# Kernel optimization log

Hardware: AMD Instinct MI355X
Metric: run time of the kernel (lower is better)

## Reference

```python
import jax, jax.numpy as jnp
import numpy as np

B, S, H, I = 2, 2048, 4096, 16384
EPS = 1e-12


def setup_inputs() -> dict:
    key = jax.random.key(0)
    ks = jax.random.split(key, 8)
    w_scale = 0.02
    return {
        "input": jax.random.normal(ks[0], (B, S, H), jnp.float32),
        "residual": jax.random.normal(ks[1], (B, S, H), jnp.float32),
        "bias": jax.random.normal(ks[2], (H,), jnp.float32) * w_scale,
        "attn_nw": jnp.ones((H,), jnp.float32),
        "attn_nb": jnp.zeros((H,), jnp.float32),
        "inter_w": jax.random.normal(ks[3], (I, H), jnp.float32) * w_scale,
        "inter_b": jax.random.normal(ks[4], (I,), jnp.float32) * w_scale,
        "output_w": jax.random.normal(ks[5], (H, I), jnp.float32) * w_scale,
        "output_b": jax.random.normal(ks[6], (H,), jnp.float32) * w_scale,
    }


def reference(input, residual, bias, attn_nw, attn_nb, inter_w, inter_b, output_w, output_b):
    # Fused mlp_gemm: residual_add = input + residual + attn-output bias
    residual_add = input + residual + bias  # [B,S,H]
    # LayerNorm over hidden dim with attn_nw/attn_nb
    mean = jnp.mean(residual_add, axis=-1, keepdims=True)
    var = jnp.var(residual_add, axis=-1, keepdims=True)
    ln = (residual_add - mean) * jax.lax.rsqrt(var + EPS) * attn_nw + attn_nb
    # Intermediate GEMM + bias + GELU (DeepSpeed uses tanh-approx gelu)
    inter = jax.nn.gelu(jnp.einsum("bsh,ih->bsi", ln, inter_w) + inter_b, approximate=True)
    # Output projection (vector_matmul)
    out = jnp.einsum("bsi,hi->bsh", inter, output_w)
    # bias_residual: add residual_add and output bias
    return out + residual_add + output_b
```

## Files before the change

### kernel.cpp

```cpp
#include <hip/hip_runtime.h>
#include <hip/hip_bf16.h>
#include <cstdint>
#include <math.h>

typedef __attribute__((ext_vector_type(4))) float f32x4;
typedef __attribute__((ext_vector_type(8))) __bf16 bf16x8;

__device__ __forceinline__ unsigned short f2bf(float f) {
    union { float f; unsigned u; } v; v.f = f;
    unsigned u = v.u + 0x7fffu + ((v.u >> 16) & 1u);
    return (unsigned short)(u >> 16);
}

__device__ __forceinline__ float gelu_tanh(float x) {
    float x3 = x * x * x;
    float t = tanhf(0.7978845608028654f * (x + 0.044715f * x3));
    return 0.5f * x * (1.0f + t);
}

__device__ __forceinline__ void gload_lds16(const void* g, void* l) {
    __builtin_amdgcn_global_load_lds(
        (__attribute__((address_space(1))) void*)(uintptr_t)g,
        (__attribute__((address_space(3))) void*)(unsigned)(uintptr_t)l,
        16, 0, 0);
}

__global__ __launch_bounds__(256)
void fused_add_ln(const float* __restrict__ in, const float* __restrict__ res,
                  const float* __restrict__ bias, const float* __restrict__ nw,
                  const float* __restrict__ nb, float* __restrict__ resadd,
                  unsigned short* __restrict__ lnout, int H) {
    const int row = blockIdx.x;
    const int tid = threadIdx.x;
    const size_t base = (size_t)row * H;
    float v[16];
    float s = 0.f, ss = 0.f;
#pragma unroll
    for (int i = 0; i < 4; ++i) {
        int idx = (i * 256 + tid) * 4;
        float4 a = *(const float4*)(in + base + idx);
        float4 b = *(const float4*)(res + base + idx);
        float4 c = *(const float4*)(bias + idx);
        float x0 = a.x + b.x + c.x, x1 = a.y + b.y + c.y;
        float x2 = a.z + b.z + c.z, x3 = a.w + b.w + c.w;
        v[i * 4 + 0] = x0; v[i * 4 + 1] = x1; v[i * 4 + 2] = x2; v[i * 4 + 3] = x3;
        s += x0 + x1 + x2 + x3;
        ss += x0 * x0 + x1 * x1 + x2 * x2 + x3 * x3;
    }
#pragma unroll
    for (int off = 32; off > 0; off >>= 1) {
        s += __shfl_down(s, off);
        ss += __shfl_down(ss, off);
    }
    __shared__ float red[8];
    const int w = tid >> 6;
    if ((tid & 63) == 0) { red[w] = s; red[4 + w] = ss; }
    __syncthreads();
    s = red[0] + red[1] + red[2] + red[3];
    ss = red[4] + red[5] + red[6] + red[7];
    const float mean = s / H;
    const float var = ss / H - mean * mean;
    const float rstd = rsqrtf(var + 1e-12f);
#pragma unroll
    for (int i = 0; i < 4; ++i) {
        int idx = (i * 256 + tid) * 4;
        float4 wv = *(const float4*)(nw + idx);
        float4 bv = *(const float4*)(nb + idx);
        float4 r;
        r.x = v[i * 4 + 0]; r.y = v[i * 4 + 1]; r.z = v[i * 4 + 2]; r.w = v[i * 4 + 3];
        *(float4*)(resadd + base + idx) = r;
        ushort4 o;
        o.x = f2bf((r.x - mean) * rstd * wv.x + bv.x);
        o.y = f2bf((r.y - mean) * rstd * wv.y + bv.y);
        o.z = f2bf((r.z - mean) * rstd * wv.z + bv.z);
        o.w = f2bf((r.w - mean) * rstd * wv.w + bv.w);
        *(ushort4*)(lnout + base + idx) = o;
    }
}

__global__ __launch_bounds__(256)
void cast_w(const float* __restrict__ w, unsigned short* __restrict__ o, long long n4) {
    long long i = (long long)blockIdx.x * 256 + threadIdx.x;
    if (i >= n4) return;
    float4 f = *(const float4*)(w + i * 4);
    ushort4 u;
    u.x = f2bf(f.x); u.y = f2bf(f.y); u.z = f2bf(f.z); u.w = f2bf(f.w);
    *(ushort4*)(o + i * 4) = u;
}

#define GBM 256
#define GBN 256

#define STAGE(s, mat, h, T) do {                                              \
    const unsigned short* _src = ((mat) ? pB : pA)                            \
        + (size_t)((h) * 128) * K + (size_t)(T) * 64;                         \
    char* _dst = ldsc + (s) * 65536 + (mat) * 32768 + (h) * 16384 + dOff;     \
    gload_lds16(_src, _dst);                                                  \
    gload_lds16(_src + (size_t)64 * K, _dst + 8192);                          \
} while (0)

#define RD_B(s) do {                                                          \
    _Pragma("unroll")                                                         \
    for (int ni = 0; ni < 4; ++ni)                                            \
        _Pragma("unroll")                                                     \
        for (int kk = 0; kk < 2; ++kk)                                        \
            bq[ni][kk] = *(const bf16x8*)(ldsc + (s) * 65536 + 32768          \
                + ((wc * 64 + ni * 16 + lrow) << 7) + ckk[kk]);               \
} while (0)

#define RD_A(q, s) do {                                                       \
    _Pragma("unroll")                                                         \
    for (int m2 = 0; m2 < 2; ++m2)                                            \
        _Pragma("unroll")                                                     \
        for (int kk = 0; kk < 2; ++kk)                                        \
            aq[m2][kk] = *(const bf16x8*)(ldsc + (s) * 65536                  \
                + ((wr * 128 + ((q) * 2 + m2) * 16 + lrow) << 7) + ckk[kk]);  \
} while (0)

#define MF(q) do {                                                            \
    __builtin_amdgcn_s_setprio(1);                                            \
    _Pragma("unroll")                                                         \
    for (int kk = 0; kk < 2; ++kk)                                            \
        _Pragma("unroll")                                                     \
        for (int m2 = 0; m2 < 2; ++m2)                                        \
            _Pragma("unroll")                                                 \
            for (int ni = 0; ni < 4; ++ni)                                    \
                acc[(q) * 2 + m2][ni] = __builtin_amdgcn_mfma_f32_16x16x32_bf16( \
                    aq[m2][kk], bq[ni][kk], acc[(q) * 2 + m2][ni], 0, 0, 0);  \
    __builtin_amdgcn_s_setprio(0);                                            \
} while (0)

#define LG do { asm volatile("s_waitcnt lgkmcnt(0)" ::: "memory");            \
                __builtin_amdgcn_sched_barrier(0); } while (0)
#define BAR   asm volatile("s_barrier" ::: "memory")
#define GATE2 asm volatile("s_waitcnt vmcnt(2)" ::: "memory")
#define GATE0 asm volatile("s_waitcnt vmcnt(0)" ::: "memory")

template <int EPI>
__global__ __launch_bounds__(512, 2)
void gemm256(const unsigned short* __restrict__ A,
             const unsigned short* __restrict__ B,
             const float* __restrict__ bias_n,
             const float* __restrict__ resadd,
             void* __restrict__ Cout,
             int M, int N, int K) {
    __shared__ unsigned short lds[2][2][2][128 * 64];
    char* ldsc = (char*)&lds[0][0][0][0];
    const int tid = threadIdx.x;
    const int lane = tid & 63;
    const int w = tid >> 6;
    const int wr = w >> 2;
    const int wc = w & 3;

    const int nwg = gridDim.x;
    const int lg = (blockIdx.x & 7) * (nwg >> 3) + (blockIdx.x >> 3);
    const int nbx = N / GBN;
    const int brow = lg / nbx;
    const int bcol = lg % nbx;

    const int srow = tid >> 3;
    const int scol = ((((tid & 7) << 4) ^ ((srow & 7) << 4)) >> 1);
    const unsigned short* pA = A + (size_t)(brow * GBM + srow) * K + scol;
    const unsigned short* pB = B + (size_t)(bcol * GBN + srow) * K + scol;
    const int dOff = tid * 16;

    const int lrow = lane & 15;
    int ckk[2];
    ckk[0] = (((lane >> 4) << 4)) ^ ((lrow & 7) << 4);
    ckk[1] = ckk[0] ^ 64;

    f32x4 acc[8][4] = {};
    bf16x8 aq[2][2];
    bf16x8 bq[4][2];

    const int NT = K / 64;
    const int niter = NT / 2;

    STAGE(0, 1, 0, 0); STAGE(0, 1, 1, 0);
    STAGE(0, 0, 0, 0); STAGE(0, 0, 1, 0);
    STAGE(1, 1, 0, 1); STAGE(1, 1, 1, 1);
    GATE0; BAR;

    for (int i = 0; i < niter - 1; ++i) {
        const int T1 = 2 * i + 1, T2 = 2 * i + 2, T3 = 2 * i + 3;
        RD_B(0); RD_A(0, 0);        BAR; STAGE(1, 0, 0, T1); LG; MF(0);
        RD_A(1, 0);                 BAR; STAGE(1, 0, 1, T1); LG; MF(1);
        RD_A(2, 0);                 BAR; STAGE(0, 1, 0, T2); LG; MF(2);
        RD_A(3, 0); GATE2;          BAR; STAGE(0, 1, 1, T2); LG; MF(3);
        RD_B(1); RD_A(0, 1);        BAR; STAGE(0, 0, 0, T2); LG; MF(0);
        RD_A(1, 1);                 BAR; STAGE(0, 0, 1, T2); LG; MF(1);
        RD_A(2, 1);                 BAR; STAGE(1, 1, 0, T3); LG; MF(2);
        RD_A(3, 1); GATE2;          BAR; STAGE(1, 1, 1, T3); LG; MF(3);
    }
    {
        const int T1 = NT - 1;
        RD_B(0); RD_A(0, 0);        BAR; STAGE(1, 0, 0, T1); LG; MF(0);
        RD_A(1, 0);                 BAR; STAGE(1, 0, 1, T1); LG; MF(1);
        RD_A(2, 0);                 BAR;                     LG; MF(2);
        RD_A(3, 0); GATE0;          BAR;                     LG; MF(3);
        RD_B(1); RD_A(0, 1);        BAR;                     LG; MF(0);
        RD_A(1, 1);                 BAR;                     LG; MF(1);
        RD_A(2, 1);                 BAR;                     LG; MF(2);
        RD_A(3, 1);                 BAR;                     LG; MF(3);
    }

    const int c0 = bcol * GBN + wc * 64 + lrow;
    const int r0 = brow * GBM + wr * 128 + (lane >> 4) * 4;
#pragma unroll
    for (int mi = 0; mi < 8; ++mi) {
#pragma unroll
        for (int j = 0; j < 4; ++j) {
            const int row = r0 + mi * 16 + j;
#pragma unroll
            for (int ni = 0; ni < 4; ++ni) {
                const int col = c0 + ni * 16;
                float x = acc[mi][ni][j] + bias_n[col];
                if (EPI == 0) {
                    ((unsigned short*)Cout)[(size_t)row * N + col] = f2bf(gelu_tanh(x));
                } else {
                    const size_t off = (size_t)row * N + col;
                    ((float*)Cout)[off] = x + resadd[off];
                }
            }
        }
    }
}

extern "C" void kernel_launch(void* const* d_in, const int* in_sizes, int n_in,
                              void* d_out, int out_size, void* d_ws, size_t ws_size,
                              hipStream_t stream) {
    const float* input    = (const float*)d_in[0];
    const float* residual = (const float*)d_in[1];
    const float* bias     = (const float*)d_in[2];
    const float* attn_nw  = (const float*)d_in[3];
    const float* attn_nb  = (const float*)d_in[4];
    const float* inter_w  = (const float*)d_in[5];
    const float* inter_b  = (const float*)d_in[6];
    const float* output_w = (const float*)d_in[7];
    const float* output_b = (const float*)d_in[8];

    const int H = in_sizes[3];
    const int I = in_sizes[6];
    const int T = in_sizes[0] / H;

    char* ws = (char*)d_ws;
    float* resadd      = (float*)ws;
    unsigned short* ln = (unsigned short*)(ws + (size_t)T * H * 4);
    unsigned short* w1 = (unsigned short*)((char*)ln + (size_t)T * H * 2);
    unsigned short* w2 = w1 + (size_t)I * H;
    unsigned short* act = w2 + (size_t)H * I;

    fused_add_ln<<<T, 256, 0, stream>>>(input, residual, bias, attn_nw, attn_nb,
                                        resadd, ln, H);

    {
        long long n4 = (long long)I * H / 4;
        int blocks = (int)((n4 + 255) / 256);
        cast_w<<<blocks, 256, 0, stream>>>(inter_w, w1, n4);
        cast_w<<<blocks, 256, 0, stream>>>(output_w, w2, n4);
    }

    {
        dim3 grid((T / GBM) * (I / GBN));
        gemm256<0><<<grid, 512, 0, stream>>>(ln, w1, inter_b, nullptr, act, T, I, H);
    }

    {
        dim3 grid((T / GBM) * (H / GBN));
        gemm256<1><<<grid, 512, 0, stream>>>(act, w2, output_b, resadd, d_out, T, H, I);
    }
}
```

Before: 1.098 ms.

## Split LDS reads per k-half and restructure GEMM stage prefetch schedule

Splits the LDS fragment reads and MFMA blocks into two k-halves so the first half of the MFMAs can begin after a partial lgkmcnt wait while the second half's reads are still in flight. It also reorders the global-to-LDS staging: the B tile for the next stage is no longer prefetched in the prologue but issued one phase later alongside A, with full vmcnt(0) gates placed earlier in the phase sequence. The intent is to overlap LDS latency with MFMA issue. In exchange, global prefetch depth shrinks, which may expose memory latency, and the hard-coded lgkmcnt counts must match the compiler's instruction order.

```diff
diff --git a/kernel.cpp b/kernel.cpp
--- a/kernel.cpp
+++ b/kernel.cpp
@@ -99,42 +99,51 @@
     gload_lds16(_src + (size_t)64 * K, _dst + 8192);                          \
 } while (0)
 
-#define RD_B(s) do {                                                          \
+#define RD_B_K(kkv, s) do {                                                   \
     _Pragma("unroll")                                                         \
     for (int ni = 0; ni < 4; ++ni)                                            \
-        _Pragma("unroll")                                                     \
-        for (int kk = 0; kk < 2; ++kk)                                        \
-            bq[ni][kk] = *(const bf16x8*)(ldsc + (s) * 65536 + 32768          \
-                + ((wc * 64 + ni * 16 + lrow) << 7) + ckk[kk]);               \
-} while (0)
-
-#define RD_A(q, s) do {                                                       \
+        bq[ni][kkv] = *(const bf16x8*)(ldsc + (s) * 65536 + 32768             \
+            + ((wc * 64 + ni * 16 + lrow) << 7) + ckk[kkv]);                  \
+} while (0)
+
+#define RD_A_K(kkv, q, s) do {                                                \
+    _Pragma("unroll")                                                         \
+    for (int m2 = 0; m2 < 2; ++m2)                                            \
+        aq[m2][kkv] = *(const bf16x8*)(ldsc + (s) * 65536                     \
+            + ((wr * 128 + ((q) * 2 + m2) * 16 + lrow) << 7) + ckk[kkv]);     \
+} while (0)
+
+#define MF_K(q, kkv) do {                                                     \
+    __builtin_amdgcn_s_setprio(1);                                            \
     _Pragma("unroll")                                                         \
     for (int m2 = 0; m2 < 2; ++m2)                                            \
         _Pragma("unroll")                                                     \
-        for (int kk = 0; kk < 2; ++kk)                                        \
-            aq[m2][kk] = *(const bf16x8*)(ldsc + (s) * 65536                  \
-                + ((wr * 128 + ((q) * 2 + m2) * 16 + lrow) << 7) + ckk[kk]);  \
-} while (0)
-
-#define MF(q) do {                                                            \
-    __builtin_amdgcn_s_setprio(1);                                            \
-    _Pragma("unroll")                                                         \
-    for (int kk = 0; kk < 2; ++kk)                                            \
-        _Pragma("unroll")                                                     \
-        for (int m2 = 0; m2 < 2; ++m2)                                        \
-            _Pragma("unroll")                                                 \
-            for (int ni = 0; ni < 4; ++ni)                                    \
-                acc[(q) * 2 + m2][ni] = __builtin_amdgcn_mfma_f32_16x16x32_bf16( \
-                    aq[m2][kk], bq[ni][kk], acc[(q) * 2 + m2][ni], 0, 0, 0);  \
+        for (int ni = 0; ni < 4; ++ni)                                        \
+            acc[(q) * 2 + m2][ni] = __builtin_amdgcn_mfma_f32_16x16x32_bf16(  \
+                aq[m2][kkv], bq[ni][kkv], acc[(q) * 2 + m2][ni], 0, 0, 0);    \
     __builtin_amdgcn_s_setprio(0);                                            \
 } while (0)
 
-#define LG do { asm volatile("s_waitcnt lgkmcnt(0)" ::: "memory");            \
-                __builtin_amdgcn_sched_barrier(0); } while (0)
+#define LGW(n) do { asm volatile("s_waitcnt lgkmcnt(" #n ")" ::: "memory");   \
+                    __builtin_amdgcn_sched_barrier(0); } while (0)
+#define SB0   __builtin_amdgcn_sched_barrier(0)
 #define BAR   asm volatile("s_barrier" ::: "memory")
-#define GATE2 asm volatile("s_waitcnt vmcnt(2)" ::: "memory")
 #define GATE0 asm volatile("s_waitcnt vmcnt(0)" ::: "memory")
+
+#define PH_Q0(s, STGS) do {                                                   \
+    RD_B_K(0, s); RD_A_K(0, 0, s); SB0;                                       \
+    RD_B_K(1, s); RD_A_K(1, 0, s); BAR;                                       \
+    STGS;                                                                     \
+    LGW(6); MF_K(0, 0); LGW(0); MF_K(0, 1);                                   \
+} while (0)
+
+#define PH_Q(q, s, PRE, STGS) do {                                            \
+    RD_A_K(0, q, s); SB0; RD_A_K(1, q, s); PRE; BAR;                          \
+    STGS;                                                                     \
+    LGW(2); MF_K(q, 0); LGW(0); MF_K(q, 1);                                   \
+} while (0)
+
+#define NOP0
 
 template <int EPI>
 __global__ __launch_bounds__(512, 2)
@@ -178,30 +187,29 @@
 
     STAGE(0, 1, 0, 0); STAGE(0, 1, 1, 0);
     STAGE(0, 0, 0, 0); STAGE(0, 0, 1, 0);
-    STAGE(1, 1, 0, 1); STAGE(1, 1, 1, 1);
     GATE0; BAR;
 
     for (int i = 0; i < niter - 1; ++i) {
-        const int T1 = 2 * i + 1, T2 = 2 * i + 2, T3 = 2 * i + 3;
-        RD_B(0); RD_A(0, 0);        BAR; STAGE(1, 0, 0, T1); LG; MF(0);
-        RD_A(1, 0);                 BAR; STAGE(1, 0, 1, T1); LG; MF(1);
-        RD_A(2, 0);                 BAR; STAGE(0, 1, 0, T2); LG; MF(2);
-        RD_A(3, 0); GATE2;          BAR; STAGE(0, 1, 1, T2); LG; MF(3);
-        RD_B(1); RD_A(0, 1);        BAR; STAGE(0, 0, 0, T2); LG; MF(0);
-        RD_A(1, 1);                 BAR; STAGE(0, 0, 1, T2); LG; MF(1);
-        RD_A(2, 1);                 BAR; STAGE(1, 1, 0, T3); LG; MF(2);
-        RD_A(3, 1); GATE2;          BAR; STAGE(1, 1, 1, T3); LG; MF(3);
+        const int T1 = 2 * i + 1, T2 = 2 * i + 2;
+        PH_Q0(0,        { STAGE(1, 0, 0, T1); STAGE(1, 0, 1, T1); });
+        PH_Q(1, 0, NOP0, { STAGE(1, 1, 0, T1); STAGE(1, 1, 1, T1); });
+        PH_Q(2, 0, GATE0, NOP0);
+        PH_Q(3, 0, NOP0, NOP0);
+        PH_Q0(1,        { STAGE(0, 0, 0, T2); STAGE(0, 0, 1, T2); });
+        PH_Q(1, 1, NOP0, { STAGE(0, 1, 0, T2); STAGE(0, 1, 1, T2); });
+        PH_Q(2, 1, GATE0, NOP0);
+        PH_Q(3, 1, NOP0, NOP0);
     }
     {
         const int T1 = NT - 1;
-        RD_B(0); RD_A(0, 0);        BAR; STAGE(1, 0, 0, T1); LG; MF(0);
-        RD_A(1, 0);                 BAR; STAGE(1, 0, 1, T1); LG; MF(1);
-        RD_A(2, 0);                 BAR;                     LG; MF(2);
-        RD_A(3, 0); GATE0;          BAR;                     LG; MF(3);
-        RD_B(1); RD_A(0, 1);        BAR;                     LG; MF(0);
-        RD_A(1, 1);                 BAR;                     LG; MF(1);
-        RD_A(2, 1);                 BAR;                     LG; MF(2);
-        RD_A(3, 1);                 BAR;                     LG; MF(3);
+        PH_Q0(0,        { STAGE(1, 0, 0, T1); STAGE(1, 0, 1, T1); });
+        PH_Q(1, 0, NOP0, { STAGE(1, 1, 0, T1); STAGE(1, 1, 1, T1); });
+        PH_Q(2, 0, GATE0, NOP0);
+        PH_Q(3, 0, NOP0, NOP0);
+        PH_Q0(1, NOP0);
+        PH_Q(1, 1, NOP0, NOP0);
+        PH_Q(2, 1, NOP0, NOP0);
+        PH_Q(3, 1, NOP0, NOP0);
     }
 
     const int c0 = bcol * GBN + wc * 64 + lrow;
```

Result: slower. 1.279 ms (+16.5%).

## Simplify GEMM pipeline to stage full next tile and drop explicit LDS waits

Applied to the files above, without the earlier changes.

Reworks the software pipeline of the bf16 MFMA GEMM. The prologue now preloads only tile 0, and each half-iteration stages both A and B halves of the next tile in the first two phases, then waits for them with a full vmcnt(0) before the remaining MFMA phases. The explicit lgkmcnt(0) waits and scheduling barriers before each MFMA block are removed, leaving LDS-read waits to the compiler. This cuts the in-flight prefetch depth, trading latency hiding for fewer forced waits and more scheduler freedom. It also risks races on the LDS buffers if the barrier placement no longer covers the new staging order.

```diff
diff --git a/kernel.cpp b/kernel.cpp
--- a/kernel.cpp
+++ b/kernel.cpp
@@ -130,10 +130,7 @@
     __builtin_amdgcn_s_setprio(0);                                            \
 } while (0)
 
-#define LG do { asm volatile("s_waitcnt lgkmcnt(0)" ::: "memory");            \
-                __builtin_amdgcn_sched_barrier(0); } while (0)
 #define BAR   asm volatile("s_barrier" ::: "memory")
-#define GATE2 asm volatile("s_waitcnt vmcnt(2)" ::: "memory")
 #define GATE0 asm volatile("s_waitcnt vmcnt(0)" ::: "memory")
 
 template <int EPI>
@@ -178,30 +175,35 @@
 
     STAGE(0, 1, 0, 0); STAGE(0, 1, 1, 0);
     STAGE(0, 0, 0, 0); STAGE(0, 0, 1, 0);
-    STAGE(1, 1, 0, 1); STAGE(1, 1, 1, 1);
     GATE0; BAR;
 
     for (int i = 0; i < niter - 1; ++i) {
-        const int T1 = 2 * i + 1, T2 = 2 * i + 2, T3 = 2 * i + 3;
-        RD_B(0); RD_A(0, 0);        BAR; STAGE(1, 0, 0, T1); LG; MF(0);
-        RD_A(1, 0);                 BAR; STAGE(1, 0, 1, T1); LG; MF(1);
-        RD_A(2, 0);                 BAR; STAGE(0, 1, 0, T2); LG; MF(2);
-        RD_A(3, 0); GATE2;          BAR; STAGE(0, 1, 1, T2); LG; MF(3);
-        RD_B(1); RD_A(0, 1);        BAR; STAGE(0, 0, 0, T2); LG; MF(0);
-        RD_A(1, 1);                 BAR; STAGE(0, 0, 1, T2); LG; MF(1);
-        RD_A(2, 1);                 BAR; STAGE(1, 1, 0, T3); LG; MF(2);
-        RD_A(3, 1); GATE2;          BAR; STAGE(1, 1, 1, T3); LG; MF(3);
+        const int T1 = 2 * i + 1, T2 = 2 * i + 2;
+        RD_B(0); RD_A(0, 0);        BAR; STAGE(1, 0, 0, T1);
+                                         STAGE(1, 0, 1, T1); MF(0);
+        RD_A(1, 0);                 BAR; STAGE(1, 1, 0, T1);
+                                         STAGE(1, 1, 1, T1); MF(1);
+        RD_A(2, 0); GATE0;          BAR;                     MF(2);
+        RD_A(3, 0);                 BAR;                     MF(3);
+        RD_B(1); RD_A(0, 1);        BAR; STAGE(0, 0, 0, T2);
+                                         STAGE(0, 0, 1, T2); MF(0);
+        RD_A(1, 1);                 BAR; STAGE(0, 1, 0, T2);
+                                         STAGE(0, 1, 1, T2); MF(1);
+        RD_A(2, 1); GATE0;          BAR;                     MF(2);
+        RD_A(3, 1);                 BAR;                     MF(3);
     }
     {
         const int T1 = NT - 1;
-        RD_B(0); RD_A(0, 0);        BAR; STAGE(1, 0, 0, T1); LG; MF(0);
-        RD_A(1, 0);                 BAR; STAGE(1, 0, 1, T1); LG; MF(1);
-        RD_A(2, 0);                 BAR;                     LG; MF(2);
-        RD_A(3, 0); GATE0;          BAR;                     LG; MF(3);
-        RD_B(1); RD_A(0, 1);        BAR;                     LG; MF(0);
-        RD_A(1, 1);                 BAR;                     LG; MF(1);
-        RD_A(2, 1);                 BAR;                     LG; MF(2);
-        RD_A(3, 1);                 BAR;                     LG; MF(3);
+        RD_B(0); RD_A(0, 0);        BAR; STAGE(1, 0, 0, T1);
+                                         STAGE(1, 0, 1, T1); MF(0);
+        RD_A(1, 0);                 BAR; STAGE(1, 1, 0, T1);
+                                         STAGE(1, 1, 1, T1); MF(1);
+        RD_A(2, 0); GATE0;          BAR;                     MF(2);
+        RD_A(3, 0);                 BAR;                     MF(3);
+        RD_B(1); RD_A(0, 1);        BAR;                     MF(0);
+        RD_A(1, 1);                 BAR;                     MF(1);
+        RD_A(2, 1);                 BAR;                     MF(2);
+        RD_A(3, 1);                 BAR;                     MF(3);
     }
 
     const int c0 = bcol * GBN + wc * 64 + lrow;
```

Result: slower. 1.288 ms (+17.2%).
